# Kernel tuning notes

Hardware: AMD Instinct MI355X
Metric: run time of the kernel (lower is better)

## Reference

```python
import jax, jax.numpy as jnp
import numpy as np

D_STATE = 16
D_CONV = 4

def layernorm(x, g, b, eps=1e-5):
    m = jnp.mean(x, -1, keepdims=True)
    v = jnp.var(x, -1, keepdims=True)
    return (x - m) / jnp.sqrt(v + eps) * g + b

def conv1x1(x, w):  # x [b,h,w,cin], w [cin,cout]
    return jnp.einsum('bhwc,cd->bhwd', x, w)

def dwconv3x3(x, w):  # x [b,h,w,C], w [3,3,1,C] (HWIO, groups=C)
    return jax.lax.conv_general_dilated(x, w, (1, 1), 'SAME',
        dimension_numbers=('NHWC', 'HWIO', 'NHWC'),
        feature_group_count=x.shape[-1])

def causal_dwconv1d(x, w, b):  # x [B,L,D], w [K,1,D]; causal depthwise conv (Mamba d_conv=4)
    xp = jnp.pad(x, ((0, 0), (D_CONV - 1, 0), (0, 0)))
    y = jax.lax.conv_general_dilated(xp, w, (1,), 'VALID',
        dimension_numbers=('NWC', 'WIO', 'NWC'),
        feature_group_count=x.shape[-1])
    return y + b

def selective_scan(deltaA, deltaBx, C):
    # deltaA, deltaBx: [B,L,D,S]; C: [B,L,S] -> y: [B,L,D]
    def step(h, inp):
        dA, dBx, c = inp
        h = dA * h + dBx
        return h, jnp.einsum('bds,bs->bd', h, c)
    h0 = jnp.zeros(deltaA.shape[:1] + deltaA.shape[2:], deltaA.dtype)
    _, ys = jax.lax.scan(step, h0,
        (jnp.swapaxes(deltaA, 0, 1), jnp.swapaxes(deltaBx, 0, 1), jnp.swapaxes(C, 0, 1)))
    return jnp.swapaxes(ys, 0, 1)

def spa_ssm(x, in_w, conv_w, conv_b, xproj_w, dt_w, dt_b, Alog, D, out_w):
    # Mamba (slow path) applied to flattened spatial sequence; x: [b,h,w,c]
    b, h, w, c = x.shape
    L = h * w
    xs = x.reshape(b, L, c)
    di = Alog.shape[0]
    xz = xs @ in_w                       # [b,L,2*di]
    xi, z = xz[..., :di], xz[..., di:]
    xi = jax.nn.silu(causal_dwconv1d(xi, conv_w, conv_b))
    dbc = xi @ xproj_w                   # [b,L,dt_rank+2*S]
    dtr = dt_w.shape[0]
    dt = jax.nn.softplus(dbc[..., :dtr] @ dt_w + dt_b)   # [b,L,di]
    B = dbc[..., dtr:dtr + D_STATE]
    C = dbc[..., dtr + D_STATE:]
    A = -jnp.exp(Alog)                   # [di,S]
    deltaA = jnp.exp(dt[..., None] * A)                  # [b,L,di,S]
    deltaBx = (dt * xi)[..., None] * B[:, :, None, :]    # [b,L,di,S]
    y = selective_scan(deltaA, deltaBx, C) + D * xi
    y = y * jax.nn.silu(z)
    return (y @ out_w).reshape(b, h, w, c)

def camba_forward(x, ln1_g, ln1_b, vin_w1, vin_dw, vin_w2, vout_dw1, vout_dw2,
                  ssm_in_w, ssm_conv_w, ssm_conv_b, ssm_xproj_w, ssm_dt_w, ssm_dt_b,
                  ssm_Alog, ssm_D, ssm_out_w, ln2_g, ln2_b, ff_w1, ff_dw, ff_w2):
    x = jnp.transpose(x, (0, 2, 3, 1))   # [b,h,w,c]
    # ESSM: v_in_head = LN -> 1x1 -> dw3x3 -> GELU -> 1x1
    x0 = conv1x1(layernorm(x, ln1_g, ln1_b), vin_w1)
    x0 = jax.nn.gelu(dwconv3x3(x0, vin_dw), approximate=False)
    x0 = conv1x1(x0, vin_w2)
    y = spa_ssm(x0, ssm_in_w, ssm_conv_w, ssm_conv_b, ssm_xproj_w,
                ssm_dt_w, ssm_dt_b, ssm_Alog, ssm_D, ssm_out_w) + x0
    # v_out_head = dw3x3 -> GELU -> dw3x3, residual
    y = dwconv3x3(jax.nn.gelu(dwconv3x3(y, vout_dw1), approximate=False), vout_dw2) + y
    x = y + x                            # block residual
    # PreNorm FeedForward (mult=4): 1x1 -> LReLU -> dw3x3 -> LReLU -> 1x1
    t = layernorm(x, ln2_g, ln2_b)
    t = jax.nn.leaky_relu(conv1x1(t, ff_w1), 0.2)
    t = jax.nn.leaky_relu(dwconv3x3(t, ff_dw), 0.2)
    t = conv1x1(t, ff_w2)
    x = t + x
    return jnp.transpose(x, (0, 3, 1, 2))

def setup_inputs() -> dict:
    key = jax.random.key(0)
    ks = jax.random.split(key, 16)
    b, c, h, w = 8, 64, 64, 64
    di, ds, dtr = 128, 16, 4
    s = 0.05
    n = lambda k, shp: jax.random.normal(k, shp, jnp.float32) * s
    dt0 = jnp.exp(jax.random.uniform(ks[1], (di,)) * (np.log(0.1) - np.log(1e-3)) + np.log(1e-3))
    return dict(
        x=jax.random.normal(ks[0], (b, c, h, w), jnp.float32),
        ln1_g=jnp.ones(c), ln1_b=jnp.zeros(c),
        vin_w1=n(ks[2], (c, c)), vin_dw=n(ks[3], (3, 3, 1, c)), vin_w2=n(ks[4], (c, c)),
        vout_dw1=n(ks[5], (3, 3, 1, c)), vout_dw2=n(ks[6], (3, 3, 1, c)),
        ssm_in_w=n(ks[7], (c, 2 * di)),
        ssm_conv_w=n(ks[8], (D_CONV, 1, di)), ssm_conv_b=jnp.zeros(di),
        ssm_xproj_w=n(ks[9], (di, dtr + 2 * ds)),
        ssm_dt_w=n(ks[10], (dtr, di)), ssm_dt_b=jnp.log(jnp.expm1(dt0)),
        ssm_Alog=jnp.log(jnp.broadcast_to(jnp.arange(1., ds + 1), (di, ds))),
        ssm_D=jnp.ones(di),
        ssm_out_w=n(ks[11], (di, c)),
        ln2_g=jnp.ones(c), ln2_b=jnp.zeros(c),
        ff_w1=n(ks[12], (c, 4 * c)), ff_dw=n(ks[13], (3, 3, 1, 4 * c)), ff_w2=n(ks[14], (4 * c, c)),
    )

def reference(x, ln1_g, ln1_b, vin_w1, vin_dw, vin_w2, vout_dw1, vout_dw2,
              ssm_in_w, ssm_conv_w, ssm_conv_b, ssm_xproj_w, ssm_dt_w, ssm_dt_b,
              ssm_Alog, ssm_D, ssm_out_w, ln2_g, ln2_b, ff_w1, ff_dw, ff_w2):
    return camba_forward(x, ln1_g, ln1_b, vin_w1, vin_dw, vin_w2, vout_dw1, vout_dw2,
                         ssm_in_w, ssm_conv_w, ssm_conv_b, ssm_xproj_w, ssm_dt_w, ssm_dt_b,
                         ssm_Alog, ssm_D, ssm_out_w, ln2_g, ln2_b, ff_w1, ff_dw, ff_w2)
```

## Files before the change

kernel.cpp:

```cpp
#include <hip/hip_runtime.h>
#include <hip/hip_bf16.h>
#include <math.h>

typedef unsigned short u16;
typedef __attribute__((ext_vector_type(8))) short s8v;
typedef __attribute__((ext_vector_type(4))) float f4v;

#define B_    8
#define C_    64
#define HW_   4096
#define NPIX  32768
#define DI    128
#define NCH   256
#define CHL   16

__device__ __forceinline__ float b2f(u16 v){ return __uint_as_float(((unsigned)v)<<16); }
__device__ __forceinline__ u16 f2b(float x){
  unsigned u = __float_as_uint(x);
  u += 0x7fff + ((u >> 16) & 1);
  return (u16)(u >> 16);
}
__device__ __forceinline__ float gelu_exact(float x){ return 0.5f*x*(1.0f+erff(x*0.70710678118654752f)); }
__device__ __forceinline__ float leaky02(float x){ return x>0.f ? x : 0.2f*x; }
__device__ __forceinline__ float softplus_(float x){ return fmaxf(x,0.f)+log1pf(__expf(-fabsf(x))); }
__device__ __forceinline__ float silu_(float x){ return x / (1.0f + __expf(-x)); }

__global__ void k_prep(const float* __restrict__ vin_w1, const float* __restrict__ vin_w2,
                       const float* __restrict__ ssm_in_w, const float* __restrict__ xproj,
                       const float* __restrict__ dtw, const float* __restrict__ ssm_outw,
                       const float* __restrict__ ff_w1, const float* __restrict__ ff_w2,
                       u16* __restrict__ wv1, u16* __restrict__ wv2, u16* __restrict__ wsi,
                       u16* __restrict__ wdb, u16* __restrict__ wout, u16* __restrict__ wf1,
                       u16* __restrict__ wf2t){
  int g = blockIdx.x*256 + threadIdx.x;
  if(g < 4096){
    int n=g>>6, c=g&63;
    wv1[n*64+c]=f2b(vin_w1[c*64+n]);
    wv2[n*64+c]=f2b(vin_w2[c*64+n]);
  }
  if(g < 16384){
    int n=g>>6, c=g&63;
    wsi[n*64+c]=f2b(ssm_in_w[c*256+n]);
    wf1[n*64+c]=f2b(ff_w1[c*256+n]);
    int n2=g/256, k2=g%256;
    wf2t[n2*256+k2]=f2b(ff_w2[k2*64+n2]);
  }
  if(g < 8192){
    int n=g>>7, k=g&127;
    wout[n*128+k]=f2b(ssm_outw[k*64+n]);
  }
  if(g < 20480){
    int n=g/128, k=g%128;
    float v;
    if(n < 128){
      v = 0.f;
      for(int r=0;r<4;r++) v += xproj[k*36+r]*dtw[r*128+n];
    }else{
      v = xproj[k*36+4+(n-128)];
    }
    wdb[n*128+k]=f2b(v);
  }
}

__global__ __launch_bounds__(256) void k_trans_ln_mm(const float* __restrict__ x,
                     const float* __restrict__ g, const float* __restrict__ bta,
                     const u16* __restrict__ wT,
                     u16* __restrict__ xT, u16* __restrict__ outp){
  const int LDA = 72, NS = 4;
  __shared__ float tile[64][65];
  __shared__ __align__(16) u16 sA[64*LDA];
  __shared__ __align__(16) u16 sW[64*LDA];
  int tid = threadIdx.x;
  int blk = blockIdx.x;
  int b = blk >> 6;
  int hwb = (blk & 63) << 6;
  int lane = tid & 63, row = tid >> 6;
  const float* src = x + (size_t)b*C_*HW_;
  #pragma unroll
  for(int k=0;k<16;k++){
    int c = row + 4*k;
    tile[c][lane] = src[c*HW_ + hwb + lane];
  }
  for(int idx=tid; idx<64*8; idx+=256){
    int n = idx>>3, c8 = (idx&7)*8;
    *(uint4*)(sW + n*LDA + c8) = *(const uint4*)(wT + n*64 + c8);
  }
  __syncthreads();
  u16* dstT = xT + (size_t)b*HW_*C_;
  #pragma unroll
  for(int k=0;k<16;k++){
    int hwl = row + 4*k;
    dstT[(hwb+hwl)*C_ + lane] = f2b(tile[lane][hwl]);
  }
  float gg = g[lane], bb = bta[lane];
  #pragma unroll
  for(int i=0;i<16;i++){
    int hwl = row*16 + i;
    float v = tile[lane][hwl];
    float s = v, sq = v*v;
    #pragma unroll
    for(int o=32;o>0;o>>=1){ s += __shfl_xor(s,o); sq += __shfl_xor(sq,o); }
    float m = s*(1.f/64.f);
    float var = sq*(1.f/64.f) - m*m;
    float r = rsqrtf(var + 1e-5f);
    sA[hwl*LDA + lane] = f2b((v-m)*r*gg + bb);
  }
  __syncthreads();
  int ln = tid & 63, wv = tid >> 6;
  int mrow = ln & 15, quad = ln >> 4;
  f4v acc[NS];
  #pragma unroll
  for(int i=0;i<NS;i++) acc[i] = (f4v){0.f,0.f,0.f,0.f};
  const u16* aBase = sA + (wv*16 + mrow)*LDA + quad*8;
  const u16* wBase = sW + mrow*LDA + quad*8;
  #pragma unroll
  for(int kk=0; kk<64; kk+=32){
    s8v af = *(const s8v*)(aBase + kk);
    #pragma unroll
    for(int ns=0; ns<NS; ns++){
      s8v bf = *(const s8v*)(wBase + ns*16*LDA + kk);
      acc[ns] = __builtin_amdgcn_mfma_f32_16x16x32_bf16(af, bf, acc[ns], 0, 0, 0);
    }
  }
  int p0 = blk*64;
  int pr = p0 + wv*16 + quad*4;
  #pragma unroll
  for(int ns=0; ns<NS; ns++){
    int n = ns*16 + mrow;
    #pragma unroll
    for(int r=0;r<4;r++)
      outp[(size_t)(pr+r)*64 + n] = f2b(acc[ns][r]);
  }
}

template<int CIN, int COUT, int ACT, bool OUTF32>
__global__ __launch_bounds__(256) void k_mfma(const u16* __restrict__ wT,
                     const u16* __restrict__ in, const float* __restrict__ bias,
                     const u16* __restrict__ res, void* __restrict__ outv){
  const int KCH = (CIN < 128) ? CIN : 128;
  const int LDA = KCH + 8;
  const int NS  = COUT / 16;
  __shared__ __align__(16) u16 sA[64*LDA];
  __shared__ __align__(16) u16 sW[COUT*LDA];
  int tid = threadIdx.x;
  int p0 = blockIdx.x * 64;
  int ln = tid & 63, wv = tid >> 6;
  int mrow = ln & 15, quad = ln >> 4;
  f4v acc[NS];
  #pragma unroll
  for(int i=0;i<NS;i++) acc[i] = (f4v){0.f,0.f,0.f,0.f};
  const u16* aBase = sA + (wv*16 + mrow)*LDA + quad*8;
  const u16* wBase = sW + mrow*LDA + quad*8;
  const int RW = KCH/8;
  for(int k0=0; k0<CIN; k0+=KCH){
    if(k0) __syncthreads();
    for(int idx=tid; idx<COUT*RW; idx+=256){
      int n = idx/RW, c8 = (idx%RW)*8;
      *(uint4*)(sW + n*LDA + c8) = *(const uint4*)(wT + (size_t)n*CIN + k0 + c8);
    }
    for(int g=tid; g<64*RW; g+=256){
      int row = g / RW, c8 = (g % RW)*8;
      *(uint4*)(sA + row*LDA + c8) = *(const uint4*)(in + (size_t)(p0+row)*CIN + k0 + c8);
    }
    __syncthreads();
    #pragma unroll
    for(int kk=0; kk<KCH; kk+=32){
      s8v af = *(const s8v*)(aBase + kk);
      #pragma unroll
      for(int ns=0; ns<NS; ns++){
        s8v bf = *(const s8v*)(wBase + ns*16*LDA + kk);
        acc[ns] = __builtin_amdgcn_mfma_f32_16x16x32_bf16(af, bf, acc[ns], 0, 0, 0);
      }
    }
  }
  int pr = p0 + wv*16 + quad*4;
  #pragma unroll
  for(int ns=0; ns<NS; ns++){
    int n = ns*16 + mrow;
    float bs = bias ? bias[n] : 0.f;
    #pragma unroll
    for(int r=0;r<4;r++){
      float v = acc[ns][r] + bs;
      if(ACT==1) v = leaky02(v);
      else if(ACT==2) v = softplus_(v);
      if(res) v += b2f(res[(size_t)(pr+r)*COUT + n]);
      if(OUTF32) ((float*)outv)[(size_t)(pr+r)*COUT + n] = v;
      else       ((u16*)outv)[(size_t)(pr+r)*COUT + n] = f2b(v);
    }
  }
}

__global__ __launch_bounds__(256) void k_mfma_ssm(const u16* __restrict__ wT,
                     const u16* __restrict__ x0,
                     const float* __restrict__ cw, const float* __restrict__ cb,
                     u16* __restrict__ xi, u16* __restrict__ zs){
  const int CIN=64, COUT=256, LDA=72, NS=16;
  __shared__ __align__(16) u16 sA[64*LDA];
  __shared__ __align__(16) u16 sW[COUT*LDA];
  __shared__ __align__(16) u16 ubuf[67*128];
  int tid = threadIdx.x;
  int p0 = blockIdx.x*64;
  int ln = tid & 63, wv = tid >> 6;
  int mrow = ln & 15, quad = ln >> 4;
  for(int idx=tid; idx<COUT*8; idx+=256){
    int n = idx>>3, c8 = (idx&7)*8;
    *(uint4*)(sW + n*LDA + c8) = *(const uint4*)(wT + n*64 + c8);
  }
  for(int g=tid; g<64*8; g+=256){
    int row = g >> 3, c8 = (g & 7)*8;
    *(uint4*)(sA + row*LDA + c8) = *(const uint4*)(x0 + (size_t)(p0+row)*64 + c8);
  }
  __syncthreads();
  f4v acc[NS];
  #pragma unroll
  for(int i=0;i<NS;i++) acc[i] = (f4v){0.f,0.f,0.f,0.f};
  const u16* aBase = sA + (wv*16 + mrow)*LDA + quad*8;
  const u16* wBase = sW + mrow*LDA + quad*8;
  #pragma unroll
  for(int kk=0; kk<CIN; kk+=32){
    s8v af = *(const s8v*)(aBase + kk);
    #pragma unroll
    for(int ns=0; ns<NS; ns++){
      s8v bf = *(const s8v*)(wBase + ns*16*LDA + kk);
      acc[ns] = __builtin_amdgcn_mfma_f32_16x16x32_bf16(af, bf, acc[ns], 0, 0, 0);
    }
  }
  bool bstart = ((p0 & 4095) == 0);
  for(int idx=tid; idx<384; idx+=256){
    int j = idx >> 7, n = idx & 127;
    float a2 = 0.f;
    if(!bstart){
      const u16* xr = x0 + (size_t)(p0-3+j)*64;
      #pragma unroll 8
      for(int c=0;c<64;c++) a2 += b2f(xr[c]) * b2f(sW[n*LDA+c]);
    }
    ubuf[j*128 + n] = f2b(a2);
  }
  int prl = wv*16 + quad*4;
  #pragma unroll
  for(int ns=0; ns<NS; ns++){
    int n = ns*16 + mrow;
    if(n < 128){
      #pragma unroll
      for(int r=0;r<4;r++) ubuf[(prl+r+3)*128 + n] = f2b(acc[ns][r]);
    }else{
      #pragma unroll
      for(int r=0;r<4;r++) zs[(size_t)(p0+prl+r)*128 + (n-128)] = f2b(silu_(acc[ns][r]));
    }
  }
  __syncthreads();
  int d4 = tid & 31;
  float4 cbv = *(const float4*)(cb + d4*4);
  for(int row = tid >> 5; row < 64; row += 8){
    float a0=cbv.x, a1=cbv.y, a2=cbv.z, a3=cbv.w;
    #pragma unroll
    for(int k=0;k<4;k++){
      ushort4 v = *(const ushort4*)(ubuf + (row+k)*128 + d4*4);
      float4 wv4 = *(const float4*)(cw + k*128 + d4*4);
      a0 += b2f(v.x)*wv4.x; a1 += b2f(v.y)*wv4.y;
      a2 += b2f(v.z)*wv4.z; a3 += b2f(v.w)*wv4.w;
    }
    ushort4 o; o.x=f2b(silu_(a0)); o.y=f2b(silu_(a1)); o.z=f2b(silu_(a2)); o.w=f2b(silu_(a3));
    *(ushort4*)(xi + (size_t)(p0+row)*128 + d4*4) = o;
  }
}

__global__ __launch_bounds__(256) void k_dtbc_scan(const u16* __restrict__ wT,
                     const u16* __restrict__ in, const float* __restrict__ dtbias,
                     const float* __restrict__ alog,
                     u16* __restrict__ dtout, u16* __restrict__ bcout,
                     u16* __restrict__ Pb, u16* __restrict__ Qb){
  const int CIN=128, COUT=160, LDA=136, NS=10;
  __shared__ __align__(16) u16 sA[64*LDA];
  __shared__ __align__(16) u16 sW[COUT*LDA];
  u16* sdt = sW;
  u16* sbc = sW + 64*128;
  int tid = threadIdx.x;
  int p0 = blockIdx.x * 64;
  int ln = tid & 63, wv = tid >> 6;
  int mrow = ln & 15, quad = ln >> 4;
  for(int idx=tid; idx<COUT*16; idx+=256){
    int n = idx>>4, c8 = (idx&15)*8;
    *(uint4*)(sW + n*LDA + c8) = *(const uint4*)(wT + n*128 + c8);
  }
  for(int g=tid; g<64*16; g+=256){
    int row = g >> 4, c8 = (g & 15)*8;
    *(uint4*)(sA + row*LDA + c8) = *(const uint4*)(in + (size_t)(p0+row)*128 + c8);
  }
  __syncthreads();
  f4v acc[NS];
  #pragma unroll
  for(int i=0;i<NS;i++) acc[i] = (f4v){0.f,0.f,0.f,0.f};
  const u16* aBase = sA + (wv*16 + mrow)*LDA + quad*8;
  const u16* wBase = sW + mrow*LDA + quad*8;
  #pragma unroll
  for(int kk=0; kk<CIN; kk+=32){
    s8v af = *(const s8v*)(aBase + kk);
    #pragma unroll
    for(int ns=0; ns<NS; ns++){
      s8v bf = *(const s8v*)(wBase + ns*16*LDA + kk);
      acc[ns] = __builtin_amdgcn_mfma_f32_16x16x32_bf16(af, bf, acc[ns], 0, 0, 0);
    }
  }
  __syncthreads();
  int pr = p0 + wv*16 + quad*4;
  int prl = wv*16 + quad*4;
  #pragma unroll
  for(int ns=0; ns<NS; ns++){
    int n = ns*16 + mrow;
    if(n < 128){
      float bs = dtbias[n];
      #pragma unroll
      for(int r=0;r<4;r++){
        u16 v = f2b(softplus_(acc[ns][r] + bs));
        dtout[(size_t)(pr+r)*128 + n] = v;
        sdt[(prl+r)*128 + n] = v;
      }
    }else{
      #pragma unroll
      for(int r=0;r<4;r++){
        u16 v = f2b(acc[ns][r]);
        bcout[(size_t)(pr+r)*32 + (n-128)] = v;
        sbc[(prl+r)*32 + (n-128)] = v;
      }
    }
  }
  __syncthreads();
  int d = tid & 127;
  int b = p0 >> 12;
  int chb = (blockIdx.x & 63)*4;
  float A[16];
  #pragma unroll
  for(int s=0;s<16;s++) A[s] = -__expf(alog[d*16+s]);
  for(int cl = tid >> 7; cl < 4; cl += 2){
    float P[16], Q[16];
    #pragma unroll
    for(int s=0;s<16;s++){ P[s]=1.f; Q[s]=0.f; }
    #pragma unroll
    for(int i=0;i<CHL;i++){
      float dtv = b2f(sdt[(cl*16+i)*128 + d]);
      float xiv = b2f(sA[(cl*16+i)*LDA + d]);
      float u = dtv*xiv;
      #pragma unroll
      for(int s=0;s<16;s++){
        float a = __expf(dtv*A[s]);
        P[s] *= a;
        Q[s] = a*Q[s] + u*b2f(sbc[(cl*16+i)*32+s]);
      }
    }
    int gidx = (chb+cl)*16384 + (b*128+d)*16;
    unsigned pw[8], qw[8];
    #pragma unroll
    for(int j=0;j<8;j++){
      pw[j] = (unsigned)f2b(P[2*j]) | ((unsigned)f2b(P[2*j+1])<<16);
      qw[j] = (unsigned)f2b(Q[2*j]) | ((unsigned)f2b(Q[2*j+1])<<16);
    }
    *(uint4*)(Pb+gidx)   = make_uint4(pw[0],pw[1],pw[2],pw[3]);
    *(uint4*)(Pb+gidx+8) = make_uint4(pw[4],pw[5],pw[6],pw[7]);
    *(uint4*)(Qb+gidx)   = make_uint4(qw[0],qw[1],qw[2],qw[3]);
    *(uint4*)(Qb+gidx+8) = make_uint4(qw[4],qw[5],qw[6],qw[7]);
  }
}

__global__ void k_scan2(const u16* __restrict__ Pb, const u16* __restrict__ Qb,
                        u16* __restrict__ Hin){
  int g = blockIdx.x*64 + threadIdx.x;
  float h = 0.f;
  #pragma unroll 8
  for(int ch=0; ch<NCH; ch++){
    Hin[ch*16384 + g] = f2b(h);
    h = b2f(Pb[ch*16384 + g])*h + b2f(Qb[ch*16384 + g]);
  }
}

__global__ __launch_bounds__(128) void k_scan3_mm(const u16* __restrict__ dt, const u16* __restrict__ xi,
                        const u16* __restrict__ bc, const u16* __restrict__ zs,
                        const float* __restrict__ alog, const float* __restrict__ Dp,
                        const u16* __restrict__ Hin, const u16* __restrict__ wout,
                        const u16* __restrict__ x0, u16* __restrict__ y){
  const int LDS2 = 136, LDW = 136;
  int blk = blockIdx.x;
  int ch = blk & (NCH-1);
  int b = blk >> 8;
  int d = threadIdx.x, tid = threadIdx.x;
  __shared__ __align__(16) u16 sdt[CHL*LDS2];
  __shared__ __align__(16) u16 sxi[CHL*128], szs[CHL*128], sbc[CHL*32];
  __shared__ __align__(16) u16 sWo[64*LDW];
  for(int idx=tid; idx<64*16; idx+=128){
    int n = idx>>4, c8 = (idx&15)*8;
    *(uint4*)(sWo + n*LDW + c8) = *(const uint4*)(wout + n*128 + c8);
  }
  float A[16], h[16];
  u16 hbuf[16];
  int gidx = ch*16384 + (b*128+d)*16;
  *(uint4*)hbuf     = *(const uint4*)(Hin+gidx);
  *(uint4*)(hbuf+8) = *(const uint4*)(Hin+gidx+8);
  #pragma unroll
  for(int s=0;s<16;s++){ A[s] = -__expf(alog[d*16+s]); h[s] = b2f(hbuf[s]); }
  float Dd = Dp[d];
  int pbase = b*HW_ + ch*CHL;
  for(int idx=tid; idx<16*16; idx+=128){
    int i = idx>>4, c8 = (idx&15)*8;
    *(uint4*)(sdt + i*LDS2 + c8) = *(const uint4*)(dt + (size_t)(pbase+i)*128 + c8);
  }
  const uint4* gxi = (const uint4*)(xi + (size_t)pbase*128);
  const uint4* gzs = (const uint4*)(zs + (size_t)pbase*128);
  ((uint4*)sxi)[d]     = gxi[d];
  ((uint4*)sxi)[d+128] = gxi[d+128];
  ((uint4*)szs)[d]     = gzs[d];
  ((uint4*)szs)[d+128] = gzs[d+128];
  if(d < 64) ((uint4*)sbc)[d] = ((const uint4*)(bc + (size_t)pbase*32))[d];
  __syncthreads();
  #pragma unroll
  for(int i=0;i<CHL;i++){
    float dtv = b2f(sdt[i*LDS2+d]);
    float xiv = b2f(sxi[i*128+d]);
    float u = dtv*xiv;
    float acc = Dd*xiv;
    #pragma unroll
    for(int s=0;s<16;s++){
      float a = __expf(dtv*A[s]);
      h[s] = a*h[s] + u*b2f(sbc[i*32+s]);
      acc += h[s]*b2f(sbc[i*32+16+s]);
    }
    sdt[i*LDS2+d] = f2b(acc * b2f(szs[i*128+d]));
  }
  __syncthreads();
  int ln = tid & 63, wv = tid >> 6;
  int mrow = ln & 15, quad = ln >> 4;
  f4v acc2[2];
  acc2[0] = (f4v){0.f,0.f,0.f,0.f};
  acc2[1] = (f4v){0.f,0.f,0.f,0.f};
  #pragma unroll
  for(int kk=0; kk<128; kk+=32){
    s8v af = *(const s8v*)(sdt + mrow*LDS2 + kk + quad*8);
    #pragma unroll
    for(int ns=0; ns<2; ns++){
      int n0 = wv*32 + ns*16;
      s8v bf = *(const s8v*)(sWo + (n0+mrow)*LDW + kk + quad*8);
      acc2[ns] = __builtin_amdgcn_mfma_f32_16x16x32_bf16(af, bf, acc2[ns], 0, 0, 0);
    }
  }
  #pragma unroll
  for(int ns=0; ns<2; ns++){
    int n = wv*32 + ns*16 + mrow;
    #pragma unroll
    for(int r=0;r<4;r++){
      int px = pbase + quad*4 + r;
      y[(size_t)px*64 + n] = f2b(acc2[ns][r] + b2f(x0[(size_t)px*64 + n]));
    }
  }
}

template<int COUT, int ACT>
__global__ __launch_bounds__(256) void k_mfma_ln(const u16* __restrict__ wT,
                     const u16* __restrict__ in, const float* __restrict__ g,
                     const float* __restrict__ bta, u16* __restrict__ outp){
  const int CIN = 64, LDA = 72, NS = COUT/16;
  __shared__ __align__(16) u16 sA[64*LDA];
  __shared__ __align__(16) u16 sW[COUT*LDA];
  int tid = threadIdx.x;
  int p0 = blockIdx.x * 64;
  int ln = tid & 63, wv = tid >> 6;
  int mrow = ln & 15, quad = ln >> 4;
  for(int idx=tid; idx<COUT*8; idx+=256){
    int n = idx>>3, c8 = (idx&7)*8;
    *(uint4*)(sW + n*LDA + c8) = *(const uint4*)(wT + n*64 + c8);
  }
  float gg = g[ln], bb = bta[ln];
  #pragma unroll
  for(int i=0;i<16;i++){
    int row = wv*16 + i;
    float v = b2f(in[(size_t)(p0+row)*64 + ln]);
    float s = v, sq = v*v;
    #pragma unroll
    for(int o=32;o>0;o>>=1){ s += __shfl_xor(s,o); sq += __shfl_xor(sq,o); }
    float m = s*(1.f/64.f);
    float var = sq*(1.f/64.f) - m*m;
    float r = rsqrtf(var + 1e-5f);
    sA[row*LDA + ln] = f2b((v-m)*r*gg + bb);
  }
  __syncthreads();
  f4v acc[NS];
  #pragma unroll
  for(int i=0;i<NS;i++) acc[i] = (f4v){0.f,0.f,0.f,0.f};
  const u16* aBase = sA + (wv*16 + mrow)*LDA + quad*8;
  const u16* wBase = sW + mrow*LDA + quad*8;
  #pragma unroll
  for(int kk=0; kk<CIN; kk+=32){
    s8v af = *(const s8v*)(aBase + kk);
    #pragma unroll
    for(int ns=0; ns<NS; ns++){
      s8v bf = *(const s8v*)(wBase + ns*16*LDA + kk);
      acc[ns] = __builtin_amdgcn_mfma_f32_16x16x32_bf16(af, bf, acc[ns], 0, 0, 0);
    }
  }
  int pr = p0 + wv*16 + quad*4;
  #pragma unroll
  for(int ns=0; ns<NS; ns++){
    int n = ns*16 + mrow;
    #pragma unroll
    for(int r=0;r<4;r++){
      float v = acc[ns][r];
      if(ACT==1) v = leaky02(v);
      outp[(size_t)(pr+r)*COUT + n] = f2b(v);
    }
  }
}

__global__ __launch_bounds__(256) void k_mfma_fin(const u16* __restrict__ wT,
                     const u16* __restrict__ in, const u16* __restrict__ res,
                     float* __restrict__ outp){
  const int CIN=256, COUT=64, KCH=128, LDA=136, NS=4;
  __shared__ __align__(16) u16 sA[64*LDA];
  __shared__ __align__(16) u16 sW[COUT*LDA];
  int tid = threadIdx.x;
  int p0 = blockIdx.x * 64;
  int ln = tid & 63, wv = tid >> 6;
  int mrow = ln & 15, quad = ln >> 4;
  f4v acc[NS];
  #pragma unroll
  for(int i=0;i<NS;i++) acc[i] = (f4v){0.f,0.f,0.f,0.f};
  const u16* aBase = sA + (wv*16 + mrow)*LDA + quad*8;
  const u16* wBase = sW + mrow*LDA + quad*8;
  for(int k0=0; k0<CIN; k0+=KCH){
    if(k0) __syncthreads();
    for(int idx=tid; idx<COUT*16; idx+=256){
      int n = idx>>4, c8 = (idx&15)*8;
      *(uint4*)(sW + n*LDA + c8) = *(const uint4*)(wT + n*256 + k0 + c8);
    }
    for(int g=tid; g<64*16; g+=256){
      int row = g >> 4, c8 = (g & 15)*8;
      *(uint4*)(sA + row*LDA + c8) = *(const uint4*)(in + (size_t)(p0+row)*CIN + k0 + c8);
    }
    __syncthreads();
    #pragma unroll
    for(int kk=0; kk<KCH; kk+=32){
      s8v af = *(const s8v*)(aBase + kk);
      #pragma unroll
      for(int ns=0; ns<NS; ns++){
        s8v bf = *(const s8v*)(wBase + ns*16*LDA + kk);
        acc[ns] = __builtin_amdgcn_mfma_f32_16x16x32_bf16(af, bf, acc[ns], 0, 0, 0);
      }
    }
  }
  int pr = p0 + wv*16 + quad*4;
  int b = blockIdx.x >> 6;
  int hwr = ((blockIdx.x & 63) << 6) + wv*16 + quad*4;
  #pragma unroll
  for(int ns=0; ns<NS; ns++){
    int n = ns*16 + mrow;
    float4 v4;
    v4.x = acc[ns][0] + b2f(res[(size_t)(pr+0)*64 + n]);
    v4.y = acc[ns][1] + b2f(res[(size_t)(pr+1)*64 + n]);
    v4.z = acc[ns][2] + b2f(res[(size_t)(pr+2)*64 + n]);
    v4.w = acc[ns][3] + b2f(res[(size_t)(pr+3)*64 + n]);
    *(float4*)(outp + (size_t)b*C_*HW_ + (size_t)n*HW_ + hwr) = v4;
  }
}

template<int CN, int ACT>
__global__ void k_dw3(const u16* __restrict__ in, const float* __restrict__ wgt,
                      const u16* __restrict__ res1, const u16* __restrict__ res2,
                      u16* __restrict__ out){
  const int C4 = CN/4;
  int g = blockIdx.x*256 + threadIdx.x;
  int c4 = g % C4;
  int pix = g / C4;
  int w = pix & 63;
  int h = (pix >> 6) & 63;
  int b = pix >> 12;
  float a0=0.f, a1=0.f, a2=0.f, a3=0.f;
  #pragma unroll
  for(int kh=0;kh<3;kh++){
    int hh = h + kh - 1;
    if((unsigned)hh < 64u){
      #pragma unroll
      for(int kw=0;kw<3;kw++){
        int ww = w + kw - 1;
        if((unsigned)ww < 64u){
          ushort4 v = *(const ushort4*)(in + (size_t)((b*64+hh)*64 + ww)*CN + c4*4);
          float4 wv = *(const float4*)(wgt + (kh*3+kw)*CN + c4*4);
          a0 += b2f(v.x)*wv.x; a1 += b2f(v.y)*wv.y;
          a2 += b2f(v.z)*wv.z; a3 += b2f(v.w)*wv.w;
        }
      }
    }
  }
  if(ACT==1){ a0=leaky02(a0); a1=leaky02(a1); a2=leaky02(a2); a3=leaky02(a3); }
  else if(ACT==2){ a0=gelu_exact(a0); a1=gelu_exact(a1); a2=gelu_exact(a2); a3=gelu_exact(a3); }
  size_t ob = (size_t)pix*CN + c4*4;
  if(res1){ ushort4 r = *(const ushort4*)(res1 + ob);
            a0+=b2f(r.x); a1+=b2f(r.y); a2+=b2f(r.z); a3+=b2f(r.w); }
  if(res2){ ushort4 r = *(const ushort4*)(res2 + ob);
            a0+=b2f(r.x); a1+=b2f(r.y); a2+=b2f(r.z); a3+=b2f(r.w); }
  ushort4 o; o.x=f2b(a0); o.y=f2b(a1); o.z=f2b(a2); o.w=f2b(a3);
  *(ushort4*)(out + ob) = o;
}

extern "C" void kernel_launch(void* const* d_in, const int* in_sizes, int n_in,
                              void* d_out, int out_size, void* d_ws, size_t ws_size,
                              hipStream_t stream) {
  const float* x        = (const float*)d_in[0];
  const float* ln1_g    = (const float*)d_in[1];
  const float* ln1_b    = (const float*)d_in[2];
  const float* vin_w1   = (const float*)d_in[3];
  const float* vin_dw   = (const float*)d_in[4];
  const float* vin_w2   = (const float*)d_in[5];
  const float* vout_dw1 = (const float*)d_in[6];
  const float* vout_dw2 = (const float*)d_in[7];
  const float* ssm_in_w = (const float*)d_in[8];
  const float* ssm_cw   = (const float*)d_in[9];
  const float* ssm_cb   = (const float*)d_in[10];
  const float* ssm_xprj = (const float*)d_in[11];
  const float* ssm_dtw  = (const float*)d_in[12];
  const float* ssm_dtb  = (const float*)d_in[13];
  const float* ssm_Alog = (const float*)d_in[14];
  const float* ssm_D    = (const float*)d_in[15];
  const float* ssm_outw = (const float*)d_in[16];
  const float* ln2_g    = (const float*)d_in[17];
  const float* ln2_b    = (const float*)d_in[18];
  const float* ff_w1    = (const float*)d_in[19];
  const float* ff_dw    = (const float*)d_in[20];
  const float* ff_w2    = (const float*)d_in[21];
  float* out = (float*)d_out;

  const size_t M = 1u<<20;
  u16* U   = (u16*)d_ws;
  u16* xT  = U;
  u16* tA  = U + 2*M;
  u16* tB  = U + 4*M;
  u16* x0  = U + 6*M;
  u16* xi  = U + 8*M;
  u16* zs  = U + 12*M;
  u16* xz  = U + 16*M;
  u16* dtb = U + 24*M;
  u16* bc  = U + 28*M;
  u16* Pb  = U + 16*M;
  u16* Qb  = U + 20*M;
  u16* Hin = tA;
  u16* y   = U + 16*M;
  u16* t2  = dtb;
  u16* wv1  = U + 33*M;
  u16* wv2  = wv1 + 4096;
  u16* wsi  = wv2 + 4096;
  u16* wdb  = wsi + 16384;
  u16* wout = wdb + 20480;
  u16* wf1  = wout + 8192;
  u16* wf2t = wf1 + 16384;

  k_prep<<<80,256,0,stream>>>(vin_w1, vin_w2, ssm_in_w, ssm_xprj, ssm_dtw, ssm_outw,
                              ff_w1, ff_w2, wv1, wv2, wsi, wdb, wout, wf1, wf2t);

  k_trans_ln_mm<<<512,256,0,stream>>>(x, ln1_g, ln1_b, wv1, xT, tB);
  k_dw3<64,2><<<2048,256,0,stream>>>(tB, vin_dw, nullptr, nullptr, tA);
  k_mfma<64,64,0,false><<<512,256,0,stream>>>(wv2, tA, nullptr, nullptr, x0);

  k_mfma_ssm<<<512,256,0,stream>>>(wsi, x0, ssm_cw, ssm_cb, xi, zs);
  k_dtbc_scan<<<512,256,0,stream>>>(wdb, xi, ssm_dtb, ssm_Alog, dtb, bc, Pb, Qb);
  k_scan2<<<256,64,0,stream>>>(Pb, Qb, Hin);
  k_scan3_mm<<<2048,128,0,stream>>>(dtb, xi, bc, zs, ssm_Alog, ssm_D, Hin, wout, x0, y);

  k_dw3<64,2><<<2048,256,0,stream>>>(y, vout_dw1, nullptr, nullptr, tA);
  k_dw3<64,0><<<2048,256,0,stream>>>(tA, vout_dw2, y, xT, x0);

  k_mfma_ln<256,1><<<512,256,0,stream>>>(wf1, x0, ln2_g, ln2_b, xz);
  k_dw3<256,1><<<8192,256,0,stream>>>(xz, ff_dw, nullptr, nullptr, t2);
  k_mfma_fin<<<512,256,0,stream>>>(wf2t, t2, x0, out);
}
```

Before: 294.6 us.

## K-chunk dt/BC weight staging, vectorize B/C LDS reads, pack scan2 pairs

k_dtbc_scan now stages the weight tile in two 64-wide K chunks, which shrinks its shared-memory footprint so more blocks can be resident per CU, at the cost of an extra barrier and reload. The scan loops in k_dtbc_scan and k_scan3_mm read B/C from LDS as 128-bit vectors and unpack them once per timestep, instead of issuing scalar 16-bit loads inside the state loop. k_scan2 handles two state lanes per thread with 32-bit loads and stores and launches half as many blocks, which lowers parallelism in that serial kernel. The sdt/sbc aliasing of sW must still fit in the smaller buffer (64*128+64*32 = 10240 u16 is under 160*72 = 11520), so it does.

```diff
diff --git a/kernel.cpp b/kernel.cpp
--- a/kernel.cpp
+++ b/kernel.cpp
@@ -24,6 +24,14 @@
 __device__ __forceinline__ float leaky02(float x){ return x>0.f ? x : 0.2f*x; }
 __device__ __forceinline__ float softplus_(float x){ return fmaxf(x,0.f)+log1pf(__expf(-fabsf(x))); }
 __device__ __forceinline__ float silu_(float x){ return x / (1.0f + __expf(-x)); }
+__device__ __forceinline__ void unpack16(uint4 q0, uint4 q1, float* v){
+  unsigned w[8]={q0.x,q0.y,q0.z,q0.w,q1.x,q1.y,q1.z,q1.w};
+  #pragma unroll
+  for(int j=0;j<8;j++){
+    v[2*j]   = __uint_as_float(w[j]<<16);
+    v[2*j+1] = __uint_as_float(w[j]&0xffff0000u);
+  }
+}
 
 __global__ void k_prep(const float* __restrict__ vin_w1, const float* __restrict__ vin_w2,
                        const float* __restrict__ ssm_in_w, const float* __restrict__ xproj,
@@ -270,36 +278,37 @@
                      const float* __restrict__ alog,
                      u16* __restrict__ dtout, u16* __restrict__ bcout,
                      u16* __restrict__ Pb, u16* __restrict__ Qb){
-  const int CIN=128, COUT=160, LDA=136, NS=10;
+  const int CIN=128, COUT=160, KCH=64, LDW=72, LDA=136, NS=10;
   __shared__ __align__(16) u16 sA[64*LDA];
-  __shared__ __align__(16) u16 sW[COUT*LDA];
+  __shared__ __align__(16) u16 sW[COUT*LDW];
   u16* sdt = sW;
   u16* sbc = sW + 64*128;
   int tid = threadIdx.x;
   int p0 = blockIdx.x * 64;
   int ln = tid & 63, wv = tid >> 6;
   int mrow = ln & 15, quad = ln >> 4;
-  for(int idx=tid; idx<COUT*16; idx+=256){
-    int n = idx>>4, c8 = (idx&15)*8;
-    *(uint4*)(sW + n*LDA + c8) = *(const uint4*)(wT + n*128 + c8);
-  }
   for(int g=tid; g<64*16; g+=256){
     int row = g >> 4, c8 = (g & 15)*8;
     *(uint4*)(sA + row*LDA + c8) = *(const uint4*)(in + (size_t)(p0+row)*128 + c8);
   }
-  __syncthreads();
   f4v acc[NS];
   #pragma unroll
   for(int i=0;i<NS;i++) acc[i] = (f4v){0.f,0.f,0.f,0.f};
-  const u16* aBase = sA + (wv*16 + mrow)*LDA + quad*8;
-  const u16* wBase = sW + mrow*LDA + quad*8;
-  #pragma unroll
-  for(int kk=0; kk<CIN; kk+=32){
-    s8v af = *(const s8v*)(aBase + kk);
-    #pragma unroll
-    for(int ns=0; ns<NS; ns++){
-      s8v bf = *(const s8v*)(wBase + ns*16*LDA + kk);
-      acc[ns] = __builtin_amdgcn_mfma_f32_16x16x32_bf16(af, bf, acc[ns], 0, 0, 0);
+  for(int k0=0; k0<CIN; k0+=KCH){
+    if(k0) __syncthreads();
+    for(int idx=tid; idx<COUT*8; idx+=256){
+      int n = idx>>3, c8 = (idx&7)*8;
+      *(uint4*)(sW + n*LDW + c8) = *(const uint4*)(wT + n*128 + k0 + c8);
+    }
+    __syncthreads();
+    #pragma unroll
+    for(int kk=0; kk<KCH; kk+=32){
+      s8v af = *(const s8v*)(sA + (wv*16+mrow)*LDA + k0 + kk + quad*8);
+      #pragma unroll
+      for(int ns=0; ns<NS; ns++){
+        s8v bf = *(const s8v*)(sW + (ns*16+mrow)*LDW + kk + quad*8);
+        acc[ns] = __builtin_amdgcn_mfma_f32_16x16x32_bf16(af, bf, acc[ns], 0, 0, 0);
+      }
     }
   }
   __syncthreads();
@@ -338,6 +347,9 @@
     for(int s=0;s<16;s++){ P[s]=1.f; Q[s]=0.f; }
     #pragma unroll
     for(int i=0;i<CHL;i++){
+      float Bv[16];
+      unpack16(*(const uint4*)(sbc + (cl*16+i)*32),
+               *(const uint4*)(sbc + (cl*16+i)*32 + 8), Bv);
       float dtv = b2f(sdt[(cl*16+i)*128 + d]);
       float xiv = b2f(sA[(cl*16+i)*LDA + d]);
       float u = dtv*xiv;
@@ -345,7 +357,7 @@
       for(int s=0;s<16;s++){
         float a = __expf(dtv*A[s]);
         P[s] *= a;
-        Q[s] = a*Q[s] + u*b2f(sbc[(cl*16+i)*32+s]);
+        Q[s] = a*Q[s] + u*Bv[s];
       }
     }
     int gidx = (chb+cl)*16384 + (b*128+d)*16;
@@ -364,12 +376,15 @@
 
 __global__ void k_scan2(const u16* __restrict__ Pb, const u16* __restrict__ Qb,
                         u16* __restrict__ Hin){
-  int g = blockIdx.x*64 + threadIdx.x;
-  float h = 0.f;
+  int g2 = (blockIdx.x*64 + threadIdx.x)*2;
+  float h0 = 0.f, h1 = 0.f;
   #pragma unroll 8
   for(int ch=0; ch<NCH; ch++){
-    Hin[ch*16384 + g] = f2b(h);
-    h = b2f(Pb[ch*16384 + g])*h + b2f(Qb[ch*16384 + g]);
+    unsigned p = *(const unsigned*)(Pb + ch*16384 + g2);
+    unsigned q = *(const unsigned*)(Qb + ch*16384 + g2);
+    *(unsigned*)(Hin + ch*16384 + g2) = (unsigned)f2b(h0) | ((unsigned)f2b(h1)<<16);
+    h0 = __uint_as_float(p<<16)*h0 + __uint_as_float(q<<16);
+    h1 = __uint_as_float(p&0xffff0000u)*h1 + __uint_as_float(q&0xffff0000u);
   }
 }
 
@@ -413,6 +428,9 @@
   __syncthreads();
   #pragma unroll
   for(int i=0;i<CHL;i++){
+    float Bv[16], Cv[16];
+    unpack16(*(const uint4*)(sbc + i*32),      *(const uint4*)(sbc + i*32 + 8),  Bv);
+    unpack16(*(const uint4*)(sbc + i*32 + 16), *(const uint4*)(sbc + i*32 + 24), Cv);
     float dtv = b2f(sdt[i*LDS2+d]);
     float xiv = b2f(sxi[i*128+d]);
     float u = dtv*xiv;
@@ -420,8 +438,8 @@
     #pragma unroll
     for(int s=0;s<16;s++){
       float a = __expf(dtv*A[s]);
-      h[s] = a*h[s] + u*b2f(sbc[i*32+s]);
-      acc += h[s]*b2f(sbc[i*32+16+s]);
+      h[s] = a*h[s] + u*Bv[s];
+      acc += h[s]*Cv[s];
     }
     sdt[i*LDS2+d] = f2b(acc * b2f(szs[i*128+d]));
   }
@@ -658,7 +676,7 @@
 
   k_mfma_ssm<<<512,256,0,stream>>>(wsi, x0, ssm_cw, ssm_cb, xi, zs);
   k_dtbc_scan<<<512,256,0,stream>>>(wdb, xi, ssm_dtb, ssm_Alog, dtb, bc, Pb, Qb);
-  k_scan2<<<256,64,0,stream>>>(Pb, Qb, Hin);
+  k_scan2<<<128,64,0,stream>>>(Pb, Qb, Hin);
   k_scan3_mm<<<2048,128,0,stream>>>(dtb, xi, bc, zs, ssm_Alog, ssm_D, Hin, wout, x0, y);
 
   k_dw3<64,2><<<2048,256,0,stream>>>(y, vout_dw1, nullptr, nullptr, tA);
```

Result: no change. 295.7 us (+0.4%).
